# Kernel optimization log

Measured on AMD Instinct MI355X. Metric: run time of the kernel, lower is better.

## Reference

```python
import jax, jax.numpy as jnp
import numpy as np

K = 1024
H = 128

def setup_inputs() -> dict:
    key = jax.random.key(0)
    ks = jax.random.split(key, 11)
    s = lambda fan_in: 1.0 / np.sqrt(fan_in)
    # coord_mlp: Linear(H, H//2) -> GELU -> Linear(H//2, 2)
    cW1 = jax.random.uniform(ks[0], (H, H // 2), minval=-s(H), maxval=s(H))
    cb1 = jax.random.uniform(ks[1], (H // 2,), minval=-s(H), maxval=s(H))
    cW2 = jax.random.uniform(ks[2], (H // 2, 2), minval=-s(H // 2), maxval=s(H // 2))
    cb2 = jax.random.uniform(ks[3], (2,), minval=-s(H // 2), maxval=s(H // 2))
    # edge_mlp: Linear(2H, H) -> GELU -> Linear(H, H//2) -> GELU -> Linear(H//2, 1)
    eW1 = jax.random.uniform(ks[4], (2 * H, H), minval=-s(2 * H), maxval=s(2 * H))
    eb1 = jax.random.uniform(ks[5], (H,), minval=-s(2 * H), maxval=s(2 * H))
    eW2 = jax.random.uniform(ks[6], (H, H // 2), minval=-s(H), maxval=s(H))
    eb2 = jax.random.uniform(ks[7], (H // 2,), minval=-s(H), maxval=s(H))
    eW3 = jax.random.uniform(ks[8], (H // 2, 1), minval=-s(H // 2), maxval=s(H // 2))
    eb3 = jax.random.uniform(ks[9], (1,), minval=-s(H // 2), maxval=s(H // 2))
    z_s = jax.random.normal(ks[10], (K, H), dtype=jnp.float32)
    return {"z_s": z_s, "cW1": cW1, "cb1": cb1, "cW2": cW2, "cb2": cb2,
            "eW1": eW1, "eb1": eb1, "eW2": eW2, "eb2": eb2, "eW3": eW3, "eb3": eb3}

def reference(z_s, cW1, cb1, cW2, cb2, eW1, eb1, eW2, eb2, eW3, eb3):
    gelu = lambda x: jax.nn.gelu(x, approximate=False)  # torch default GELU is exact erf form
    # coords: [k, 2]
    coords_pred = gelu(z_s @ cW1 + cb1) @ cW2 + cb2
    # edge first layer: cat([zi, zj]) @ eW1 == zi @ eW1[:H] + zj @ eW1[H:]
    # (same math as the broadcast-concat, without materializing [k, k, 2H])
    pi = z_s @ eW1[:H]   # [k, H]
    pj = z_s @ eW1[H:]   # [k, H]
    h1 = gelu(pi[:, None, :] + pj[None, :, :] + eb1)   # [k, k, H]
    h2 = gelu(h1 @ eW2 + eb2)                          # [k, k, H//2]
    adj_logits = (h2 @ eW3 + eb3)[..., 0]              # [k, k]
    adj_logits = (adj_logits + adj_logits.T) / 2.0
    return (coords_pred, adj_logits)
```

## Files before the change

kernel.cpp:

```cpp
#include <hip/hip_runtime.h>
#include <hip/hip_fp16.h>


#define KN 1024
#define HN 128

typedef float  floatx4 __attribute__((ext_vector_type(4)));
typedef _Float16 half8v __attribute__((ext_vector_type(8)));

__device__ __forceinline__ float gelu_f(float x) {
    float x2 = x * x;
    float t  = fmaf(x2, -0.1029434f, -2.3022087f);
    float e  = __builtin_amdgcn_exp2f(x * t);
    return x * __builtin_amdgcn_rcpf(e + 1.0f);
}

__device__ __forceinline__ unsigned int gelu2u(unsigned int xu) {
    __half2 x  = __builtin_bit_cast(__half2, xu);
    __half2 x2 = __hmul2(x, x);
    __half2 t  = __hfma2(x2, __float2half2_rn(-0.1029434f),
                             __float2half2_rn(-2.3022087f));
    __half2 e  = h2exp2(__hmul2(x, t));
    __half2 r  = h2rcp(__hadd2(e, __float2half2_rn(1.0f)));
    return __builtin_bit_cast(unsigned int, __hmul2(x, r));
}

__device__ __forceinline__ unsigned int cvt2u(float a, float b) {
    return __builtin_bit_cast(unsigned int, __builtin_amdgcn_cvt_pkrtz(a, b));
}

__device__ __forceinline__ float dotw3(const floatx4* acc, half8v w3f0,
                                       half8v w3f1, float b3) {
    uint4 u0, u1;
    u0.x = gelu2u(cvt2u(acc[0][0], acc[0][1]));
    u0.y = gelu2u(cvt2u(acc[0][2], acc[0][3]));
    u0.z = gelu2u(cvt2u(acc[1][0], acc[1][1]));
    u0.w = gelu2u(cvt2u(acc[1][2], acc[1][3]));
    u1.x = gelu2u(cvt2u(acc[2][0], acc[2][1]));
    u1.y = gelu2u(cvt2u(acc[2][2], acc[2][3]));
    u1.z = gelu2u(cvt2u(acc[3][0], acc[3][1]));
    u1.w = gelu2u(cvt2u(acc[3][2], acc[3][3]));
    half8v h20 = __builtin_bit_cast(half8v, u0);
    half8v h21 = __builtin_bit_cast(half8v, u1);
    floatx4 d = (floatx4){b3, b3, b3, b3};
    d = __builtin_amdgcn_mfma_f32_16x16x32_f16(w3f0, h20, d, 0, 0, 0);
    d = __builtin_amdgcn_mfma_f32_16x16x32_f16(w3f1, h21, d, 0, 0, 0);
    return d[0];
}

__global__ __launch_bounds__(512) void prep_kernel(
    const float* __restrict__ z,   const float* __restrict__ cW1,
    const float* __restrict__ cb1, const float* __restrict__ cW2,
    const float* __restrict__ cb2, const float* __restrict__ eW1,
    const float* __restrict__ eb1, const float* __restrict__ eW2,
    const float* __restrict__ eW3,
    _Float16* __restrict__ pi_h,   _Float16* __restrict__ pj_h,
    _Float16* __restrict__ w2T,    _Float16* __restrict__ w3h,
    float* __restrict__ coords ) {
    __shared__ float z16[16][128];
    __shared__ float c1s[16][64];
    const int tid = threadIdx.x;
    const int r0  = blockIdx.x * 16;

    if (blockIdx.x < 16) {
        int e = blockIdx.x * 512 + tid;
        int d = e >> 7, k = e & 127;
        int R = ((d >> 5) & 1) * 32 + ((d >> 2) & 1) * 16 +
                ((d >> 3) & 3) * 4  + (d & 3);
        w2T[R * 128 + k] = (_Float16)eW2[k * 64 + d];
    }
    if (blockIdx.x == 16 && tid < 64) w3h[tid] = (_Float16)eW3[tid];

#pragma unroll
    for (int s = 0; s < 4; ++s) {
        int e = tid + 512 * s;
        z16[e >> 7][e & 127] = z[r0 * HN + e];
    }
    __syncthreads();

    const int col = tid & 127, which = tid >> 7;
    const int sel = which & 1, half = which >> 1;
    const float* w = eW1 + sel * HN * HN + col;
    float acc8[8] = {0.f, 0.f, 0.f, 0.f, 0.f, 0.f, 0.f, 0.f};
    for (int k = 0; k < HN; ++k) {
        float wv = w[k * HN];
#pragma unroll
        for (int r = 0; r < 8; ++r)
            acc8[r] = fmaf(z16[half * 8 + r][k], wv, acc8[r]);
    }
    if (sel == 0) {
        float b = eb1[col];
#pragma unroll
        for (int r = 0; r < 8; ++r)
            pi_h[(r0 + half * 8 + r) * HN + col] = (_Float16)(acc8[r] + b);
    } else {
#pragma unroll
        for (int r = 0; r < 8; ++r)
            pj_h[(r0 + half * 8 + r) * HN + col] = (_Float16)acc8[r];
    }

#pragma unroll
    for (int s = 0; s < 2; ++s) {
        int task = tid + 512 * s;
        int row = task >> 6, mid = task & 63;
        float a = cb1[mid];
        for (int k = 0; k < HN; ++k) a = fmaf(z16[row][k], cW1[k * 64 + mid], a);
        c1s[row][mid] = gelu_f(a);
    }
    __syncthreads();
    if (tid < 32) {
        int row = tid >> 1, o = tid & 1;
        float a = cb2[o];
#pragma unroll 8
        for (int m = 0; m < 64; ++m) a = fmaf(c1s[row][m], cW2[m * 2 + o], a);
        coords[(r0 + row) * 2 + o] = a;
    }
}

__global__ __launch_bounds__(512, 4) void edge_kernel(
    const _Float16* __restrict__ pi_h, const _Float16* __restrict__ pj_h,
    const _Float16* __restrict__ w2T,  const _Float16* __restrict__ w3h,
    const float* __restrict__ eb2,     const float* __restrict__ eb3,
    float* __restrict__ out_adj) {
    __shared__ __align__(16) unsigned int pi_s[64 * 64];
    __shared__ __align__(16) unsigned int pj_s[32 * 64];
    __shared__ __align__(16) unsigned int w2_s[64 * 64];
    const int i0 = blockIdx.y * 64, j0 = blockIdx.x * 32;
    const int tid = threadIdx.x;

    const unsigned int* piu = (const unsigned int*)pi_h;
    const unsigned int* pju = (const unsigned int*)pj_h;
    const unsigned int* w2u = (const unsigned int*)w2T;

#pragma unroll
    for (int s = 0; s < 8; ++s) {
        int e = tid + 512 * s;
        int r = e >> 6;
        pi_s[e ^ ((r & 7) << 2)] = piu[(i0 + r) * 64 + (e & 63)];
    }
#pragma unroll
    for (int s = 0; s < 4; ++s) {
        int e = tid + 512 * s;
        int r = e >> 6;
        pj_s[e ^ ((r & 7) << 2)] = pju[(j0 + r) * 64 + (e & 63)];
    }
#pragma unroll
    for (int s = 0; s < 8; ++s) {
        int e = tid + 512 * s;
        int r = e >> 6;
        w2_s[e ^ ((r & 7) << 2)] = w2u[e];
    }

    const int lane = tid & 63;
    const int wave = tid >> 6;
    const int lrow = lane & 15;
    const int lhi  = lane >> 4;
    const int lhi4 = lhi << 2;
    const int lhi8 = lhi << 3;
    const int swzJ = (lrow & 7) << 2;

    const half8v w3f0 = *reinterpret_cast<const half8v*>(&w3h[lhi8]);
    const half8v w3f1 = *reinterpret_cast<const half8v*>(&w3h[32 + lhi8]);
    const float4 e0 = *reinterpret_cast<const float4*>(&eb2[lhi8]);
    const float4 e1 = *reinterpret_cast<const float4*>(&eb2[lhi8 + 4]);
    const float4 e2 = *reinterpret_cast<const float4*>(&eb2[32 + lhi8]);
    const float4 e3 = *reinterpret_cast<const float4*>(&eb2[36 + lhi8]);
    const float b3 = eb3[0];
    __syncthreads();

    const unsigned int* pjA = &pj_s[lrow << 6];
    const unsigned int* pjB = &pj_s[(16 + lrow) << 6];
    half8v bA[4], bB[4];
#pragma unroll
    for (int q = 0; q < 4; ++q) {
        const int ko = ((q << 4) | lhi4) ^ swzJ;
        bA[q] = *reinterpret_cast<const half8v*>(&pjA[ko]);
        bB[q] = *reinterpret_cast<const half8v*>(&pjB[ko]);
    }
    const unsigned int* w2base = &w2_s[lrow << 6];

#pragma unroll
    for (int t = 0; t < 8; ++t) {
        const int iL = (wave << 3) + t;
        const unsigned int* pirow = &pi_s[iL << 6];
        const int swzI = t << 2;

        floatx4 accA[4], accB[4];
        accA[0] = (floatx4){e0.x, e0.y, e0.z, e0.w};
        accA[1] = (floatx4){e1.x, e1.y, e1.z, e1.w};
        accA[2] = (floatx4){e2.x, e2.y, e2.z, e2.w};
        accA[3] = (floatx4){e3.x, e3.y, e3.z, e3.w};
#pragma unroll
        for (int c = 0; c < 4; ++c) accB[c] = accA[c];

#pragma unroll
        for (int q = 0; q < 4; ++q) {
            const int ko = (q << 4) | lhi4;
            half8v a = *reinterpret_cast<const half8v*>(&pirow[ko ^ swzI]);

            uint4 sA = __builtin_bit_cast(uint4, a + bA[q]);
            uint4 gA;
            gA.x = gelu2u(sA.x); gA.y = gelu2u(sA.y);
            gA.z = gelu2u(sA.z); gA.w = gelu2u(sA.w);
            half8v afA = __builtin_bit_cast(half8v, gA);

            uint4 sB = __builtin_bit_cast(uint4, a + bB[q]);
            uint4 gB;
            gB.x = gelu2u(sB.x); gB.y = gelu2u(sB.y);
            gB.z = gelu2u(sB.z); gB.w = gelu2u(sB.w);
            half8v afB = __builtin_bit_cast(half8v, gB);

            const int kw = ko ^ swzJ;
#pragma unroll
            for (int c = 0; c < 4; ++c) {
                half8v bf = *reinterpret_cast<const half8v*>(
                    &w2base[(c << 10) + kw]);
                accA[c] = __builtin_amdgcn_mfma_f32_16x16x32_f16(
                    bf, afA, accA[c], 0, 0, 0);
                accB[c] = __builtin_amdgcn_mfma_f32_16x16x32_f16(
                    bf, afB, accB[c], 0, 0, 0);
            }
        }

        const float dA = dotw3(accA, w3f0, w3f1, b3);
        const float dB = dotw3(accB, w3f0, w3f1, b3);
        if (lhi == 0) {
            float* row = &out_adj[(size_t)(i0 + iL) * KN + j0];
            row[lrow]      = dA;
            row[16 + lrow] = dB;
        }
    }
}

__global__ __launch_bounds__(256) void sym_kernel(float* __restrict__ adj) {
    int idx = blockIdx.x * 256 + threadIdx.x;
    int i = idx >> 10, j = idx & 1023;
    if (j < i) return;
    float a = adj[i * KN + j];
    float b = adj[j * KN + i];
    float m = 0.5f * (a + b);
    adj[i * KN + j] = m;
    adj[j * KN + i] = m;
}

extern "C" void kernel_launch(void* const* d_in, const int* in_sizes, int n_in,
                              void* d_out, int out_size, void* d_ws, size_t ws_size,
                              hipStream_t stream) {
    const float* z   = (const float*)d_in[0];
    const float* cW1 = (const float*)d_in[1];
    const float* cb1 = (const float*)d_in[2];
    const float* cW2 = (const float*)d_in[3];
    const float* cb2 = (const float*)d_in[4];
    const float* eW1 = (const float*)d_in[5];
    const float* eb1 = (const float*)d_in[6];
    const float* eW2 = (const float*)d_in[7];
    const float* eb2 = (const float*)d_in[8];
    const float* eW3 = (const float*)d_in[9];
    const float* eb3 = (const float*)d_in[10];

    float* out = (float*)d_out;
    _Float16* pi_h = (_Float16*)d_ws;
    _Float16* pj_h = pi_h + KN * HN;
    _Float16* w2T  = pj_h + KN * HN;
    _Float16* w3h  = w2T + 64 * HN;

    prep_kernel<<<64, 512, 0, stream>>>(z, cW1, cb1, cW2, cb2, eW1, eb1, eW2,
                                        eW3, pi_h, pj_h, w2T, w3h, out);

    dim3 gridB(32, 16);
    edge_kernel<<<gridB, 512, 0, stream>>>(pi_h, pj_h, w2T, w3h, eb2, eb3,
                                           out + 2048);

    sym_kernel<<<4096, 256, 0, stream>>>(out + 2048);
}
```

Before: 80.96 us.

## Shrink edge tiles, read pi/pj directly from global, double prep grid

The edge kernel now uses 32x32 tiles, doubling the grid to 1024 blocks, and raises the occupancy hint to 8 blocks per CU. It drops the pi/pj shared-memory staging, loading those fragments straight from global/L2 into registers, and only stages w2 in LDS using 16-byte vector copies. The prep kernel is split into 128 blocks of 256 threads handling 8 rows each. The intent is to improve occupancy and load balance and cut LDS traffic and footprint, at the cost of redundant uncached-by-LDS global reads of pi/pj rows and more w2 reloads per block.

New measurement: 122.1 us. 1.51x slower.

```diff
diff --git a/kernel.cpp b/kernel.cpp
--- a/kernel.cpp
+++ b/kernel.cpp
@@ -48,7 +48,7 @@
     return d[0];
 }
 
-__global__ __launch_bounds__(512) void prep_kernel(
+__global__ __launch_bounds__(256) void prep_kernel(
     const float* __restrict__ z,   const float* __restrict__ cW1,
     const float* __restrict__ cb1, const float* __restrict__ cW2,
     const float* __restrict__ cb2, const float* __restrict__ eW1,
@@ -57,58 +57,56 @@
     _Float16* __restrict__ pi_h,   _Float16* __restrict__ pj_h,
     _Float16* __restrict__ w2T,    _Float16* __restrict__ w3h,
     float* __restrict__ coords ) {
-    __shared__ float z16[16][128];
-    __shared__ float c1s[16][64];
+    __shared__ float z8[8][128];
+    __shared__ float c1s[8][64];
     const int tid = threadIdx.x;
-    const int r0  = blockIdx.x * 16;
-
-    if (blockIdx.x < 16) {
-        int e = blockIdx.x * 512 + tid;
+    const int r0  = blockIdx.x * 8;
+
+    if (blockIdx.x < 32) {
+        int e = blockIdx.x * 256 + tid;
         int d = e >> 7, k = e & 127;
         int R = ((d >> 5) & 1) * 32 + ((d >> 2) & 1) * 16 +
                 ((d >> 3) & 3) * 4  + (d & 3);
         w2T[R * 128 + k] = (_Float16)eW2[k * 64 + d];
     }
-    if (blockIdx.x == 16 && tid < 64) w3h[tid] = (_Float16)eW3[tid];
+    if (blockIdx.x == 32 && tid < 64) w3h[tid] = (_Float16)eW3[tid];
 
 #pragma unroll
     for (int s = 0; s < 4; ++s) {
-        int e = tid + 512 * s;
-        z16[e >> 7][e & 127] = z[r0 * HN + e];
+        int e = tid + 256 * s;
+        z8[e >> 7][e & 127] = z[r0 * HN + e];
     }
     __syncthreads();
 
     const int col = tid & 127, which = tid >> 7;
-    const int sel = which & 1, half = which >> 1;
-    const float* w = eW1 + sel * HN * HN + col;
+    const float* w = eW1 + which * HN * HN + col;
     float acc8[8] = {0.f, 0.f, 0.f, 0.f, 0.f, 0.f, 0.f, 0.f};
     for (int k = 0; k < HN; ++k) {
         float wv = w[k * HN];
 #pragma unroll
+        for (int r = 0; r < 8; ++r) acc8[r] = fmaf(z8[r][k], wv, acc8[r]);
+    }
+    if (which == 0) {
+        float b = eb1[col];
+#pragma unroll
         for (int r = 0; r < 8; ++r)
-            acc8[r] = fmaf(z16[half * 8 + r][k], wv, acc8[r]);
-    }
-    if (sel == 0) {
-        float b = eb1[col];
+            pi_h[(r0 + r) * HN + col] = (_Float16)(acc8[r] + b);
+    } else {
 #pragma unroll
         for (int r = 0; r < 8; ++r)
-            pi_h[(r0 + half * 8 + r) * HN + col] = (_Float16)(acc8[r] + b);
-    } else {
-#pragma unroll
-        for (int r = 0; r < 8; ++r)
-            pj_h[(r0 + half * 8 + r) * HN + col] = (_Float16)acc8[r];
+            pj_h[(r0 + r) * HN + col] = (_Float16)acc8[r];
     }
 
 #pragma unroll
     for (int s = 0; s < 2; ++s) {
-        int task = tid + 512 * s;
+        int task = tid + 256 * s;
         int row = task >> 6, mid = task & 63;
         float a = cb1[mid];
-        for (int k = 0; k < HN; ++k) a = fmaf(z16[row][k], cW1[k * 64 + mid], a);
+        for (int k = 0; k < HN; ++k) a = fmaf(z8[row][k], cW1[k * 64 + mid], a);
         c1s[row][mid] = gelu_f(a);
     }
     __syncthreads();
-    if (tid < 32) {
+    if (tid < 16) {
         int row = tid >> 1, o = tid & 1;
         float a = cb2[o];
 #pragma unroll 8
@@ -117,15 +115,13 @@
     }
 }
 
-__global__ __launch_bounds__(512, 4) void edge_kernel(
+__global__ __launch_bounds__(512, 8) void edge_kernel(
     const _Float16* __restrict__ pi_h, const _Float16* __restrict__ pj_h,
     const _Float16* __restrict__ w2T,  const _Float16* __restrict__ w3h,
     const float* __restrict__ eb2,     const float* __restrict__ eb3,
     float* __restrict__ out_adj) {
-    __shared__ __align__(16) unsigned int pi_s[64 * 64];
-    __shared__ __align__(16) unsigned int pj_s[32 * 64];
     __shared__ __align__(16) unsigned int w2_s[64 * 64];
-    const int i0 = blockIdx.y * 64, j0 = blockIdx.x * 32;
+    const int i0 = blockIdx.y * 32, j0 = blockIdx.x * 32;
     const int tid = threadIdx.x;
 
     const unsigned int* piu = (const unsigned int*)pi_h;
@@ -133,22 +129,11 @@
     const unsigned int* w2u = (const unsigned int*)w2T;
 
 #pragma unroll
-    for (int s = 0; s < 8; ++s) {
-        int e = tid + 512 * s;
+    for (int s = 0; s < 2; ++s) {
+        int e = tid * 4 + 2048 * s;
         int r = e >> 6;
-        pi_s[e ^ ((r & 7) << 2)] = piu[(i0 + r) * 64 + (e & 63)];
-    }
-#pragma unroll
-    for (int s = 0; s < 4; ++s) {
-        int e = tid + 512 * s;
-        int r = e >> 6;
-        pj_s[e ^ ((r & 7) << 2)] = pju[(j0 + r) * 64 + (e & 63)];
-    }
-#pragma unroll
-    for (int s = 0; s < 8; ++s) {
-        int e = tid + 512 * s;
-        int r = e >> 6;
-        w2_s[e ^ ((r & 7) << 2)] = w2u[e];
+        uint4 v = *reinterpret_cast<const uint4*>(&w2u[e]);
+        *reinterpret_cast<uint4*>(&w2_s[e ^ ((r & 7) << 2)]) = v;
     }
 
     const int lane = tid & 63;
@@ -157,7 +142,18 @@
     const int lhi  = lane >> 4;
     const int lhi4 = lhi << 2;
     const int lhi8 = lhi << 3;
-    const int swzJ = (lrow & 7) << 2;
+    const int swzW = (lrow & 7) << 2;
+
+    const unsigned int* pjA = &pju[(j0 + lrow) * 64];
+    const unsigned int* pjB = &pju[(j0 + 16 + lrow) * 64];
+    half8v bA[4], bB[4];
+#pragma unroll
+    for (int q = 0; q < 4; ++q) {
+        const int ko = (q << 4) | lhi4;
+        bA[q] = *reinterpret_cast<const half8v*>(&pjA[ko]);
+        bB[q] = *reinterpret_cast<const half8v*>(&pjB[ko]);
+    }
+    const unsigned int* w2base = &w2_s[lrow << 6];
 
     const half8v w3f0 = *reinterpret_cast<const half8v*>(&w3h[lhi8]);
     const half8v w3f1 = *reinterpret_cast<const half8v*>(&w3h[32 + lhi8]);
@@ -168,22 +164,10 @@
     const float b3 = eb3[0];
     __syncthreads();
 
-    const unsigned int* pjA = &pj_s[lrow << 6];
-    const unsigned int* pjB = &pj_s[(16 + lrow) << 6];
-    half8v bA[4], bB[4];
-#pragma unroll
-    for (int q = 0; q < 4; ++q) {
-        const int ko = ((q << 4) | lhi4) ^ swzJ;
-        bA[q] = *reinterpret_cast<const half8v*>(&pjA[ko]);
-        bB[q] = *reinterpret_cast<const half8v*>(&pjB[ko]);
-    }
-    const unsigned int* w2base = &w2_s[lrow << 6];
-
-#pragma unroll
-    for (int t = 0; t < 8; ++t) {
-        const int iL = (wave << 3) + t;
-        const unsigned int* pirow = &pi_s[iL << 6];
-        const int swzI = t << 2;
+#pragma unroll
+    for (int t = 0; t < 4; ++t) {
+        const int iL = (wave << 2) + t;
+        const unsigned int* pirow = &piu[(size_t)(i0 + iL) * 64];
 
         floatx4 accA[4], accB[4];
         accA[0] = (floatx4){e0.x, e0.y, e0.z, e0.w};
@@ -196,7 +180,7 @@
 #pragma unroll
         for (int q = 0; q < 4; ++q) {
             const int ko = (q << 4) | lhi4;
-            half8v a = *reinterpret_cast<const half8v*>(&pirow[ko ^ swzI]);
+            half8v a = *reinterpret_cast<const half8v*>(&pirow[ko]);
 
             uint4 sA = __builtin_bit_cast(uint4, a + bA[q]);
             uint4 gA;
@@ -210,7 +194,7 @@
             gB.z = gelu2u(sB.z); gB.w = gelu2u(sB.w);
             half8v afB = __builtin_bit_cast(half8v, gB);
 
-            const int kw = ko ^ swzJ;
+            const int kw = ko ^ swzW;
 #pragma unroll
             for (int c = 0; c < 4; ++c) {
                 half8v bf = *reinterpret_cast<const half8v*>(
@@ -264,10 +248,10 @@
     _Float16* w2T  = pj_h + KN * HN;
     _Float16* w3h  = w2T + 64 * HN;
 
-    prep_kernel<<<64, 512, 0, stream>>>(z, cW1, cb1, cW2, cb2, eW1, eb1, eW2,
-                                        eW3, pi_h, pj_h, w2T, w3h, out);
-
-    dim3 gridB(32, 16);
+    prep_kernel<<<128, 256, 0, stream>>>(z, cW1, cb1, cW2, cb2, eW1, eb1, eW2,
+                                         eW3, pi_h, pj_h, w2T, w3h, out);
+
+    dim3 gridB(32, 32);
     edge_kernel<<<gridB, 512, 0, stream>>>(pi_h, pj_h, w2T, w3h, eb2, eb3,
                                            out + 2048);
 
```
